# Kernel tuning notes

Measured on AMD Instinct MI355X. Metric: run time of the kernel, lower is better.

## Reference

```python
import jax, jax.numpy as jnp
import numpy as np

N_FILTERS = 40
FILTER_SIZE = 401   # int(16000*25/1000), forced odd
POOL_STRIDE = 160   # int(16000*10/1000)
EPS = 1e-6
S_SMOOTH = 0.04     # fixed PCEN smoothing coefficient s
DELTA = 2.0         # fixed PCEN bias delta
R_MIN, R_MAX = 0.2, 1.0
HIDDEN = 32


def setup_inputs() -> dict:
    key = jax.random.key(0)
    ks = jax.random.split(key, 6)
    B, L = 8, 160000
    x = jax.random.normal(ks[0], (B, L), dtype=jnp.float32)
    # mel-initialized Gabor params (as in mel_filter_params)
    sr, fmin, fmax = 16000.0, 60.0, 7800.0
    min_mel = 1127.0 * np.log1p(fmin / 700.0)
    max_mel = 1127.0 * np.log1p(fmax / 700.0)
    peaks_mel = np.linspace(min_mel, max_mel, N_FILTERS + 2)
    peaks_hz = 700.0 * np.expm1(peaks_mel / 1127.0)
    center_freqs = jnp.asarray(peaks_hz[1:-1] * 2.0 * np.pi / sr, dtype=jnp.float32)
    z = np.sqrt(2.0 * np.log(2.0)) / np.pi
    bandwidths = jnp.asarray(z * sr / (peaks_hz[2:] - peaks_hz[:-2]), dtype=jnp.float32)
    pooling_widths = jnp.full((N_FILTERS,), 0.4, dtype=jnp.float32)
    # GRU (input_size=1, hidden=32) + head Linear(32,32)->ReLU->Linear(32,2)
    def gl(k, shape):
        return jax.random.normal(k, shape, dtype=jnp.float32) * 0.1
    w_ih = gl(ks[1], (3 * HIDDEN, 1))
    w_hh = gl(ks[2], (3 * HIDDEN, HIDDEN))
    b_ih = jnp.zeros((3 * HIDDEN,), jnp.float32)
    b_hh = jnp.zeros((3 * HIDDEN,), jnp.float32)
    hw1 = gl(ks[3], (32, HIDDEN)); hb1 = jnp.zeros((32,), jnp.float32)
    hw2 = gl(ks[4], (2, 32)); hb2 = jnp.zeros((2,), jnp.float32)
    return dict(x=x, center_freqs=center_freqs, bandwidths=bandwidths,
                pooling_widths=pooling_widths, w_ih=w_ih, w_hh=w_hh,
                b_ih=b_ih, b_hh=b_hh, hw1=hw1, hb1=hb1, hw2=hw2, hb2=hb2)


def _gabor_filterbank(x, center_freqs, bandwidths, pooling_widths):
    z = np.sqrt(2.0 * np.log(2.0)) / np.pi
    cf = jnp.clip(center_freqs, 0.0, np.pi)
    bw = jnp.clip(bandwidths, 4.0 * z, FILTER_SIZE * z)
    t = jnp.arange(-(FILTER_SIZE // 2), (FILTER_SIZE + 1) // 2, dtype=jnp.float32)
    denom = 1.0 / (jnp.sqrt(2.0 * np.pi) * bw)                        # [F]
    gauss = jnp.exp(-(t[None, :] ** 2) / (2.0 * bw[:, None] ** 2))    # [F,K]
    phase = cf[:, None] * t[None, :]                                  # [F,K]
    fr = denom[:, None] * gauss * jnp.cos(phase)
    fi = denom[:, None] * gauss * jnp.sin(phase)
    filt = jnp.concatenate([fr, fi], axis=0)[:, None, :]              # [2F,1,K]
    pad = FILTER_SIZE // 2
    y = jax.lax.conv_general_dilated(x[:, None, :], filt, (1,), [(pad, pad)])
    y = y ** 2
    y = y[:, :N_FILTERS] + y[:, N_FILTERS:]                           # squared modulus [B,F,L]
    pw = jnp.clip(pooling_widths, 2.0 / FILTER_SIZE, 0.5)
    tt = jnp.arange(FILTER_SIZE, dtype=jnp.float32) / (FILTER_SIZE - 1) - 0.5
    win = jnp.exp(-0.5 * (tt[None, :] / pw[:, None]) ** 2)[:, None, :]  # [F,1,K]
    y = jax.lax.conv_general_dilated(y, win, (POOL_STRIDE,), [(pad, pad)],
                                     feature_group_count=N_FILTERS)
    return y  # [B,F,T]


def _gru_cell(h, xin, w_ih, w_hh, b_ih, b_hh):
    gi = xin @ w_ih.T + b_ih   # [N,3H]
    gh = h @ w_hh.T + b_hh
    i_r, i_z, i_n = jnp.split(gi, 3, axis=-1)
    h_r, h_z, h_n = jnp.split(gh, 3, axis=-1)
    r = jax.nn.sigmoid(i_r + h_r)
    zz = jax.nn.sigmoid(i_z + h_z)
    n = jnp.tanh(i_n + r * h_n)
    return (1.0 - zz) * n + zz * h


def _adaptive_pcen(frames, w_ih, w_hh, b_ih, b_hh, hw1, hb1, hw2, hb2):
    B, F, T = frames.shape
    Xt = jnp.transpose(frames, (2, 0, 1))  # [T,B,F]

    def controller(x_prev, x_t):  # each [B,F] -> per-bin (alpha, r)
        xp = x_prev.reshape(-1, 1)
        xc = x_t.reshape(-1, 1)
        h = jnp.zeros((B * F, HIDDEN), frames.dtype)
        h = _gru_cell(h, xp, w_ih, w_hh, b_ih, b_hh)
        h = _gru_cell(h, xc, w_ih, w_hh, b_ih, b_hh)
        hid = jax.nn.relu(h @ hw1.T + hb1)
        logits = hid @ hw2.T + hb2  # [B*F,2]
        alpha = jax.nn.sigmoid(logits[:, 0]).reshape(B, F)
        r = (R_MIN + (R_MAX - R_MIN) * jax.nn.sigmoid(logits[:, 1])).reshape(B, F)
        return alpha, r

    def step(carry, X_t):
        M_prev, X_prev = carry
        alpha, r = controller(X_prev, X_t)
        M_t = (1.0 - S_SMOOTH) * M_prev + S_SMOOTH * X_t
        out = (X_t / (M_t + EPS) ** alpha + DELTA) ** r - DELTA ** r
        return (M_t, X_t), out

    init = (jnp.zeros((B, F), frames.dtype), Xt[0])
    _, outs = jax.lax.scan(step, init, Xt)
    return jnp.transpose(outs, (1, 2, 0))  # [B,F,T]


def reference(x, center_freqs, bandwidths, pooling_widths,
              w_ih, w_hh, b_ih, b_hh, hw1, hb1, hw2, hb2):
    frames = _gabor_filterbank(x, center_freqs, bandwidths, pooling_widths)
    return _adaptive_pcen(frames, w_ih, w_hh, b_ih, b_hh, hw1, hb1, hw2, hb2)
```

## Files before the change

### kernel.cpp

```cpp
#include <hip/hip_runtime.h>
#include <math.h>

#define NF 40
#define FS 401
#define AST 424
#define PSTRIDE 160
#define BB 8
#define LL 160000
#define PADL 256
#define LST 161024
#define TOUT 1000
#define NTILE 512
#define NCHUNKC 313
#define ROWCH 121
#define ROWST (ROWCH*8)
#define EROW 520
#define TCP 16
#define NCHUNKP 63
#define NCONVB 5032

typedef __attribute__((ext_vector_type(8))) _Float16 half8v;
typedef __attribute__((ext_vector_type(4))) _Float16 half4v;
typedef __attribute__((ext_vector_type(4))) float float4v;
typedef _Float16 f16;

__device__ __forceinline__ float sigm(float x) { return 1.0f / (1.0f + __expf(-x)); }
__device__ __forceinline__ float tanh_fast(float x) { return 1.0f - 2.0f / (__expf(2.0f * x) + 1.0f); }

__global__ __launch_bounds__(256) void prep_all(
    const float* __restrict__ x, const float* __restrict__ cf_,
    const float* __restrict__ bw_, f16* __restrict__ xb, f16* __restrict__ Ag)
{
    int blk = blockIdx.x;
    if (blk < NCONVB) {
        int i = blk * 256 + threadIdx.x;
        int b = i / LST, o = i % LST;
        float v = 0.0f;
        if (o >= PADL && o < PADL + LL) v = x[b * LL + (o - PADL)];
        xb[i] = (f16)v;
        return;
    }
    const float PI_F = 3.14159265358979323846f;
    int row = blk - NCONVB;
    int f = row >> 1, comp = row & 1;
    float Z = sqrtf(2.0f * logf(2.0f)) / PI_F;
    float cf = fminf(fmaxf(cf_[f], 0.0f), PI_F);
    float bw = fminf(fmaxf(bw_[f], 4.0f * Z), 401.0f * Z);
    float denom = 1.0f / (sqrtf(2.0f * PI_F) * bw);
    float inv2 = 1.0f / (2.0f * bw * bw);
    for (int k = threadIdx.x; k < AST; k += 256) {
        float v = 0.0f;
        if (k < FS) {
            float t = (float)(k - 200);
            float g = denom * expf(-(t * t) * inv2);
            float sv, cv;
            sincosf(cf * t, &sv, &cv);
            v = comp ? g * sv : g * cv;
        }
        Ag[row * AST + k] = (f16)v;
    }
}

__global__ __launch_bounds__(256, 2) void conv_mfma(
    const f16* __restrict__ xb,
    const f16* __restrict__ Ag,
    f16* __restrict__ eb)
{
    __shared__ __align__(16) unsigned char smem[40 * EROW * 2];
    f16* slab = (f16*)smem;
    f16* eL   = (f16*)smem;

    int chunk = blockIdx.x;
    int bi = blockIdx.y;
    int p0 = chunk * NTILE;
    int pbase = PADL + p0 - 200;
    const f16* xs = xb + (size_t)bi * LST;
    int tid = threadIdx.x;

    for (int sc = tid; sc < 8 * 120; sc += 256) {
        int r = sc / 120, m = sc - r * 120;
        int s0 = pbase + 8 * m + (r & ~1);
        const uint* gp = (const uint*)(xs + s0);
        uint v0 = gp[0], v1 = gp[1], v2 = gp[2], v3 = gp[3], v4 = gp[4];
        if (r & 1) {
            v0 = __builtin_amdgcn_alignbyte(v1, v0, 2);
            v1 = __builtin_amdgcn_alignbyte(v2, v1, 2);
            v2 = __builtin_amdgcn_alignbyte(v3, v2, 2);
            v3 = __builtin_amdgcn_alignbyte(v4, v3, 2);
        }
        *(uint4*)(&slab[r * ROWST + 8 * m]) = make_uint4(v0, v1, v2, v3);
    }
    __syncthreads();

    int wv = tid >> 6, lane = tid & 63, q = lane >> 4, l15 = lane & 15;

    float4v acc[5][8];
#pragma unroll
    for (int t = 0; t < 5; ++t)
#pragma unroll
        for (int s = 0; s < 8; ++s)
            acc[t][s] = (float4v){0.f, 0.f, 0.f, 0.f};

    const f16* aP[5];
    const f16* bPtr[10];
#pragma unroll
    for (int t = 0; t < 5; ++t) aP[t] = Ag + (16 * t + l15) * AST + 8 * q;
#pragma unroll
    for (int s = 0; s < 10; ++s) {
        int pos = 128 * wv + 16 * s + l15;
        bPtr[s] = slab + (pos & 7) * ROWST + 8 * ((pos >> 3) + q);
    }

    half8v bf[8];
#pragma unroll
    for (int s = 0; s < 8; ++s) bf[s] = *(const half8v*)(bPtr[s]);

#pragma unroll
    for (int kk = 0; kk < 13; ++kk) {
        int k = 32 * kk;
        half8v af[5];
#pragma unroll
        for (int t = 0; t < 5; ++t) af[t] = *(const half8v*)(aP[t] + k);
        half8v nb0, nb1;
        if (kk < 12) {
            nb0 = *(const half8v*)(bPtr[8] + k);
            nb1 = *(const half8v*)(bPtr[9] + k);
        }
#pragma unroll
        for (int t = 0; t < 5; ++t)
#pragma unroll
            for (int s = 0; s < 8; ++s)
                acc[t][s] = __builtin_amdgcn_mfma_f32_16x16x32_f16(af[t], bf[s], acc[t][s], 0, 0, 0);
        if (kk < 12) {
#pragma unroll
            for (int s = 0; s < 6; ++s) bf[s] = bf[s + 2];
            bf[6] = nb0; bf[7] = nb1;
        }
    }

    __syncthreads();

#pragma unroll
    for (int t = 0; t < 5; ++t) {
        int f0 = 8 * t + 2 * q;
#pragma unroll
        for (int s = 0; s < 8; ++s) {
            float4v a = acc[t][s];
            int pl = 128 * wv + 16 * s + l15;
            eL[f0 * EROW + pl] = (f16)(a.x * a.x + a.y * a.y);
            eL[(f0 + 1) * EROW + pl] = (f16)(a.z * a.z + a.w * a.w);
        }
    }
    __syncthreads();

    f16* ebb = eb + (size_t)bi * NF * LL;
#pragma unroll
    for (int it = 0; it < 10; ++it) {
        int idx = it * 256 + tid;
        int row = idx >> 6;
        int off = (idx & 63) * 8;
        if (p0 + off < LL) {
            uint4 v = *(const uint4*)(&eL[row * EROW + off]);
            *(uint4*)(&ebb[row * LL + p0 + off]) = v;
        }
    }
}

__global__ __launch_bounds__(256) void pool_kernel(
    const f16* __restrict__ eb, const float* __restrict__ pw_, float* __restrict__ Xout)
{
    __shared__ float ys[2816];
    __shared__ float win[416];
    int chunk = blockIdx.x;
    int f = blockIdx.y;
    int bi = blockIdx.z;
    int tau0 = chunk * TCP;
    int start = tau0 * PSTRIDE - 200;
    int tid = threadIdx.x;

    float pw = fminf(fmaxf(pw_[f], 2.0f / 401.0f), 0.5f);
    float invpw = 1.0f / pw;
    for (int k = tid; k < 416; k += 256) {
        float w = 0.0f;
        if (k < FS) {
            float tt = (float)k * (1.0f / 400.0f) - 0.5f;
            float u = tt * invpw;
            w = expf(-0.5f * u * u);
        }
        win[k] = w;
    }
    const f16* erow = eb + ((size_t)bi * NF + f) * LL;
    if (start >= 0 && start + 2816 <= LL) {
        for (int j = tid; j < 352; j += 256) {
            half8v v = *(const half8v*)(erow + start + 8 * j);
#pragma unroll
            for (int i = 0; i < 8; ++i) ys[8 * j + i] = (float)v[i];
        }
    } else {
        for (int j = tid; j < 2816; j += 256) {
            int p = start + j;
            ys[j] = (p >= 0 && p < LL) ? (float)erow[p] : 0.0f;
        }
    }
    __syncthreads();

    int ft = tid >> 4, l16 = tid & 15;
    float acc = 0.0f;
    int yo = ft * PSTRIDE;
    for (int kw = l16; kw < FS; kw += 16)
        acc += ys[yo + kw] * win[kw];
#pragma unroll
    for (int off = 8; off > 0; off >>= 1)
        acc += __shfl_down(acc, off, 16);
    int tau = tau0 + ft;
    if (l16 == 0 && tau < TOUT)
        Xout[((size_t)bi * NF + f) * TOUT + tau] = acc;
}

__global__ __launch_bounds__(256) void pcen_scan_kernel(
    const float* __restrict__ X, float* __restrict__ M)
{
    int wid = (blockIdx.x * 256 + threadIdx.x) >> 6;
    int lane = threadIdx.x & 63;
    if (wid >= BB * NF) return;
    const float a1 = 0.96f;
    const float a2 = a1 * a1;
    const float a4 = a2 * a2;
    const float a8 = a4 * a4;
    const float a16 = a8 * a8;
    const float a32 = a16 * a16;
    const float ss = 0.04f;
    float al1 = powf(a1, (float)(lane + 1));
    float carry = 0.0f;
    const float* row = X + wid * TOUT;
    float* mrow = M + wid * TOUT;

    for (int c = 0; c < TOUT; c += 64) {
        int t = c + lane;
        float v = (t < TOUT) ? row[t] : 0.0f;
        float y = ss * v;
        float u;
        u = __shfl_up(y, 1, 64);  if (lane >= 1)  y = fmaf(a1, u, y);
        u = __shfl_up(y, 2, 64);  if (lane >= 2)  y = fmaf(a2, u, y);
        u = __shfl_up(y, 4, 64);  if (lane >= 4)  y = fmaf(a4, u, y);
        u = __shfl_up(y, 8, 64);  if (lane >= 8)  y = fmaf(a8, u, y);
        u = __shfl_up(y, 16, 64); if (lane >= 16) y = fmaf(a16, u, y);
        u = __shfl_up(y, 32, 64); if (lane >= 32) y = fmaf(a32, u, y);
        y = fmaf(al1, carry, y);
        carry = __shfl(y, 63, 64);
        if (t < TOUT) mrow[t] = y;
    }
}

__global__ __launch_bounds__(256) void pcen_ctrl_mfma(
    const float* __restrict__ X, const float* __restrict__ M,
    const float* __restrict__ w_ih, const float* __restrict__ w_hh,
    const float* __restrict__ b_ih, const float* __restrict__ b_hh,
    const float* __restrict__ hw1, const float* __restrict__ hb1,
    const float* __restrict__ hw2, const float* __restrict__ hb2,
    float* __restrict__ out)
{
    __shared__ f16 s_whhA[96 * 40];
    __shared__ f16 s_w1A[32 * 40];
    __shared__ __align__(16) float4 s_A1[32];
    __shared__ __align__(16) float4 s_A2[32];
    __shared__ float s_hb1[32];
    __shared__ float s_hw2[64];
    __shared__ float s_hb2[2];
    __shared__ f16 sh1[4][16 * 40];
    __shared__ f16 sh2[4][16 * 40];
    __shared__ float sxc[4][16], sxp[4][16], smv[4][16];

    int tid = threadIdx.x;
    for (int i = tid; i < 96 * 32; i += 256) {
        int m = i >> 5, k = i & 31;
        s_whhA[m * 40 + k] = (f16)w_hh[i];
    }
    for (int i = tid; i < 32 * 32; i += 256) {
        int m = i >> 5, k = i & 31;
        s_w1A[m * 40 + k] = (f16)hw1[i];
    }
    if (tid < 32) {
        int j = tid;
        s_A1[j] = make_float4(w_ih[j], b_ih[j] + b_hh[j],
                              w_ih[32 + j], b_ih[32 + j] + b_hh[32 + j]);
        s_A2[j] = make_float4(w_ih[64 + j], b_ih[64 + j], b_hh[64 + j], 0.0f);
        s_hb1[j] = hb1[j];
    }
    if (tid < 64) s_hw2[tid] = hw2[tid];
    if (tid < 2)  s_hb2[tid] = hb2[tid];
    __syncthreads();

    int wv = tid >> 6, lane = tid & 63;
    int c = lane & 15, q = lane >> 4;
    int instBase = blockIdx.x * 64 + wv * 16;

    if (lane < 16) {
        int idx = instBase + lane;
        int t = idx % TOUT;
        float xcv = X[idx];
        float xpv = (t == 0) ? xcv : X[idx - 1];
        sxc[wv][lane] = xcv;
        sxp[wv][lane] = xpv;
        smv[wv][lane] = M[idx];
    }
    float xp = sxp[wv][c];
    float xc = sxc[wv][c];
    float mv = smv[wv][c];

    float h1v[8];
#pragma unroll
    for (int jj = 0; jj < 8; ++jj) {
        int j = (jj < 4) ? (4 * q + jj) : (16 + 4 * q + (jj - 4));
        float4 a1 = s_A1[j];
        float4 a2 = s_A2[j];
        float r = sigm(fmaf(xp, a1.x, a1.y));
        float z = sigm(fmaf(xp, a1.z, a1.w));
        float n = tanh_fast(fmaf(xp, a2.x, a2.y) + r * a2.z);
        h1v[jj] = (1.0f - z) * n;
    }

    {
        half4v lo = {(f16)h1v[0], (f16)h1v[1], (f16)h1v[2], (f16)h1v[3]};
        half4v hi = {(f16)h1v[4], (f16)h1v[5], (f16)h1v[6], (f16)h1v[7]};
        *(half4v*)(&sh1[wv][c * 40 + 4 * q]) = lo;
        *(half4v*)(&sh1[wv][c * 40 + 16 + 4 * q]) = hi;
    }

    float4v acc[6];
    {
        half8v bf = *(const half8v*)(&sh1[wv][c * 40 + 8 * q]);
#pragma unroll
        for (int t = 0; t < 6; ++t) {
            half8v af = *(const half8v*)(&s_whhA[(16 * t + c) * 40 + 8 * q]);
            acc[t] = __builtin_amdgcn_mfma_f32_16x16x32_f16(af, bf, (float4v){0.f,0.f,0.f,0.f}, 0, 0, 0);
        }
    }

    float h2v[8];
#pragma unroll
    for (int jj = 0; jj < 8; ++jj) {
        int j = (jj < 4) ? (4 * q + jj) : (16 + 4 * q + (jj - 4));
        int reg = jj & 3;
        float accR = (jj < 4) ? acc[0][reg] : acc[1][reg];
        float accZ = (jj < 4) ? acc[2][reg] : acc[3][reg];
        float accN = (jj < 4) ? acc[4][reg] : acc[5][reg];
        float4 a1 = s_A1[j];
        float4 a2 = s_A2[j];
        float r = sigm(fmaf(xc, a1.x, a1.y) + accR);
        float z = sigm(fmaf(xc, a1.z, a1.w) + accZ);
        float gn = accN + a2.z;
        float n = tanh_fast(fmaf(xc, a2.x, a2.y) + r * gn);
        h2v[jj] = fmaf(z, h1v[jj] - n, n);
    }

    {
        half4v lo = {(f16)h2v[0], (f16)h2v[1], (f16)h2v[2], (f16)h2v[3]};
        half4v hi = {(f16)h2v[4], (f16)h2v[5], (f16)h2v[6], (f16)h2v[7]};
        *(half4v*)(&sh2[wv][c * 40 + 4 * q]) = lo;
        *(half4v*)(&sh2[wv][c * 40 + 16 + 4 * q]) = hi;
    }

    float4v hacc[2];
    {
        half8v bf = *(const half8v*)(&sh2[wv][c * 40 + 8 * q]);
#pragma unroll
        for (int t = 0; t < 2; ++t) {
            half8v af = *(const half8v*)(&s_w1A[(16 * t + c) * 40 + 8 * q]);
            hacc[t] = __builtin_amdgcn_mfma_f32_16x16x32_f16(af, bf, (float4v){0.f,0.f,0.f,0.f}, 0, 0, 0);
        }
    }

    float p0 = 0.f, p1 = 0.f;
#pragma unroll
    for (int jj = 0; jj < 8; ++jj) {
        int i = (jj < 4) ? (4 * q + jj) : (16 + 4 * q + (jj - 4));
        int reg = jj & 3;
        float hv = (jj < 4) ? hacc[0][reg] : hacc[1][reg];
        hv = fmaxf(hv + s_hb1[i], 0.0f);
        p0 = fmaf(hv, s_hw2[i], p0);
        p1 = fmaf(hv, s_hw2[32 + i], p1);
    }
    p0 += __shfl_xor(p0, 16);
    p0 += __shfl_xor(p0, 32);
    p1 += __shfl_xor(p1, 16);
    p1 += __shfl_xor(p1, 32);

    float alpha = sigm(p0 + s_hb2[0]);
    float rr = fmaf(0.8f, sigm(p1 + s_hb2[1]), 0.2f);
    float md = __expf(alpha * __logf(mv + 1e-6f));
    float bse = xc / md + 2.0f;
    float val = __expf(rr * __logf(bse)) - __expf(rr * 0.69314718056f);
    if (lane < 16)
        out[instBase + lane] = val;
}

extern "C" void kernel_launch(void* const* d_in, const int* in_sizes, int n_in,
                              void* d_out, int out_size, void* d_ws, size_t ws_size,
                              hipStream_t stream) {
    const float* x    = (const float*)d_in[0];
    const float* cf   = (const float*)d_in[1];
    const float* bw   = (const float*)d_in[2];
    const float* pw   = (const float*)d_in[3];
    const float* w_ih = (const float*)d_in[4];
    const float* w_hh = (const float*)d_in[5];
    const float* b_ih = (const float*)d_in[6];
    const float* b_hh = (const float*)d_in[7];
    const float* hw1  = (const float*)d_in[8];
    const float* hb1  = (const float*)d_in[9];
    const float* hw2  = (const float*)d_in[10];
    const float* hb2  = (const float*)d_in[11];
    float* out = (float*)d_out;

    const size_t xb_b = (size_t)BB * LST * 2;
    const size_t ag_b = (size_t)80 * AST * 2;
    const size_t xm_b = (size_t)2 * BB * NF * TOUT * 4;
    size_t fixed = xb_b + ag_b + xm_b;
    size_t e_per_batch = (size_t)NF * LL * 2;
    int nb;
    if (ws_size >= fixed + 8 * e_per_batch)      nb = 8;
    else if (ws_size >= fixed + 2 * e_per_batch) nb = 2;
    else                                         nb = 1;
    int nslice = BB / nb;

    f16* xb   = (f16*)d_ws;
    f16* Ag   = xb + (size_t)BB * LST;
    f16* ebuf = Ag + (size_t)80 * AST;
    float* Xf = (float*)(ebuf + (size_t)nb * NF * LL);
    float* Mf = Xf + (size_t)BB * NF * TOUT;

    prep_all<<<dim3(NCONVB + 80), dim3(256), 0, stream>>>(x, cf, bw, xb, Ag);

    for (int sl = 0; sl < nslice; ++sl) {
        conv_mfma<<<dim3(NCHUNKC, nb), dim3(256), 0, stream>>>(
            xb + (size_t)sl * nb * LST, Ag, ebuf);
        pool_kernel<<<dim3(NCHUNKP, NF, nb), dim3(256), 0, stream>>>(
            ebuf, pw, Xf + (size_t)sl * nb * NF * TOUT);
    }

    pcen_scan_kernel<<<dim3((BB * NF * 64) / 256), dim3(256), 0, stream>>>(Xf, Mf);
    pcen_ctrl_mfma<<<dim3((BB * NF * TOUT) / 64), dim3(256), 0, stream>>>(
        Xf, Mf, w_ih, w_hh, b_ih, b_hh, hw1, hb1, hw2, hb2, out);
}
```

Before: 260.7 us.

## Precompute pooling windows, keep pooling tiles in f16, batch more work per block

Gaussian pooling windows are now computed once per filter in the prep kernel instead of in every pooling block. The pool kernel stages the energy tile in shared memory as f16 rather than expanded float, and each block now covers 32 frames using paired half2/float2 loads. The PCEN controller kernel now handles four 16-instance groups per wave in a loop, which cuts the launch to a quarter of the blocks and amortises the shared-memory weight setup. The cost is more serial work per block and one extra small workspace buffer.

```diff
diff --git a/kernel.cpp b/kernel.cpp
--- a/kernel.cpp
+++ b/kernel.cpp
@@ -15,12 +15,15 @@
 #define ROWCH 121
 #define ROWST (ROWCH*8)
 #define EROW 520
-#define TCP 16
-#define NCHUNKP 63
+#define TCP 32
+#define NCHUNKP 32
+#define PELEM (TCP*PSTRIDE + 408)
+#define WROW 402
 #define NCONVB 5032
 
 typedef __attribute__((ext_vector_type(8))) _Float16 half8v;
 typedef __attribute__((ext_vector_type(4))) _Float16 half4v;
+typedef __attribute__((ext_vector_type(2))) _Float16 half2v;
 typedef __attribute__((ext_vector_type(4))) float float4v;
 typedef _Float16 f16;
 
@@ -29,7 +32,8 @@
 
 __global__ __launch_bounds__(256) void prep_all(
     const float* __restrict__ x, const float* __restrict__ cf_,
-    const float* __restrict__ bw_, f16* __restrict__ xb, f16* __restrict__ Ag)
+    const float* __restrict__ bw_, const float* __restrict__ pw_,
+    f16* __restrict__ xb, f16* __restrict__ Ag, float* __restrict__ winG)
 {
     int blk = blockIdx.x;
     if (blk < NCONVB) {
@@ -41,23 +45,38 @@
         return;
     }
     const float PI_F = 3.14159265358979323846f;
-    int row = blk - NCONVB;
-    int f = row >> 1, comp = row & 1;
-    float Z = sqrtf(2.0f * logf(2.0f)) / PI_F;
-    float cf = fminf(fmaxf(cf_[f], 0.0f), PI_F);
-    float bw = fminf(fmaxf(bw_[f], 4.0f * Z), 401.0f * Z);
-    float denom = 1.0f / (sqrtf(2.0f * PI_F) * bw);
-    float inv2 = 1.0f / (2.0f * bw * bw);
-    for (int k = threadIdx.x; k < AST; k += 256) {
-        float v = 0.0f;
-        if (k < FS) {
-            float t = (float)(k - 200);
-            float g = denom * expf(-(t * t) * inv2);
-            float sv, cv;
-            sincosf(cf * t, &sv, &cv);
-            v = comp ? g * sv : g * cv;
-        }
-        Ag[row * AST + k] = (f16)v;
+    if (blk < NCONVB + 80) {
+        int row = blk - NCONVB;
+        int f = row >> 1, comp = row & 1;
+        float Z = sqrtf(2.0f * logf(2.0f)) / PI_F;
+        float cf = fminf(fmaxf(cf_[f], 0.0f), PI_F);
+        float bw = fminf(fmaxf(bw_[f], 4.0f * Z), 401.0f * Z);
+        float denom = 1.0f / (sqrtf(2.0f * PI_F) * bw);
+        float inv2 = 1.0f / (2.0f * bw * bw);
+        for (int k = threadIdx.x; k < AST; k += 256) {
+            float v = 0.0f;
+            if (k < FS) {
+                float t = (float)(k - 200);
+                float g = denom * expf(-(t * t) * inv2);
+                float sv, cv;
+                sincosf(cf * t, &sv, &cv);
+                v = comp ? g * sv : g * cv;
+            }
+            Ag[row * AST + k] = (f16)v;
+        }
+        return;
+    }
+    int f = blk - NCONVB - 80;
+    float pw = fminf(fmaxf(pw_[f], 2.0f / 401.0f), 0.5f);
+    float invpw = 1.0f / pw;
+    for (int j = threadIdx.x; j < WROW; j += 256) {
+        float w = 0.0f;
+        if (j < FS) {
+            float tt = (float)j * (1.0f / 400.0f) - 0.5f;
+            float u = tt * invpw;
+            w = expf(-0.5f * u * u);
+        }
+        winG[f * WROW + j] = w;
     }
 }
 
@@ -167,10 +186,10 @@
 }
 
 __global__ __launch_bounds__(256) void pool_kernel(
-    const f16* __restrict__ eb, const float* __restrict__ pw_, float* __restrict__ Xout)
+    const f16* __restrict__ eb, const float* __restrict__ winG, float* __restrict__ Xout)
 {
-    __shared__ float ys[2816];
-    __shared__ float win[416];
+    __shared__ __align__(16) f16 es[PELEM + 8];
+    __shared__ __align__(16) float win[416];
     int chunk = blockIdx.x;
     int f = blockIdx.y;
     int bi = blockIdx.z;
@@ -178,43 +197,42 @@
     int start = tau0 * PSTRIDE - 200;
     int tid = threadIdx.x;
 
-    float pw = fminf(fmaxf(pw_[f], 2.0f / 401.0f), 0.5f);
-    float invpw = 1.0f / pw;
-    for (int k = tid; k < 416; k += 256) {
-        float w = 0.0f;
-        if (k < FS) {
-            float tt = (float)k * (1.0f / 400.0f) - 0.5f;
-            float u = tt * invpw;
-            w = expf(-0.5f * u * u);
-        }
-        win[k] = w;
-    }
+    for (int k = tid; k < 416; k += 256)
+        win[k] = (k < WROW) ? winG[f * WROW + k] : 0.0f;
+
     const f16* erow = eb + ((size_t)bi * NF + f) * LL;
-    if (start >= 0 && start + 2816 <= LL) {
-        for (int j = tid; j < 352; j += 256) {
-            half8v v = *(const half8v*)(erow + start + 8 * j);
-#pragma unroll
-            for (int i = 0; i < 8; ++i) ys[8 * j + i] = (float)v[i];
-        }
+    if (start >= 0 && start + PELEM <= LL) {
+        for (int j = tid; j < PELEM / 8; j += 256)
+            *(uint4*)(&es[8 * j]) = *(const uint4*)(erow + start + 8 * j);
     } else {
-        for (int j = tid; j < 2816; j += 256) {
+        for (int j = tid; j < PELEM; j += 256) {
             int p = start + j;
-            ys[j] = (p >= 0 && p < LL) ? (float)erow[p] : 0.0f;
+            es[j] = (p >= 0 && p < LL) ? erow[p] : (f16)0.0f;
         }
     }
     __syncthreads();
 
     int ft = tid >> 4, l16 = tid & 15;
-    float acc = 0.0f;
-    int yo = ft * PSTRIDE;
-    for (int kw = l16; kw < FS; kw += 16)
-        acc += ys[yo + kw] * win[kw];
-#pragma unroll
-    for (int off = 8; off > 0; off >>= 1)
-        acc += __shfl_down(acc, off, 16);
-    int tau = tau0 + ft;
-    if (l16 == 0 && tau < TOUT)
-        Xout[((size_t)bi * NF + f) * TOUT + tau] = acc;
+#pragma unroll
+    for (int pass = 0; pass < 2; ++pass) {
+        int frame = pass * 16 + ft;
+        int base = frame * PSTRIDE;
+        float acc = 0.0f;
+#pragma unroll
+        for (int m = 0; m < 13; ++m) {
+            int kw = 2 * l16 + 32 * m;
+            half2v ep = *(const half2v*)(&es[base + kw]);
+            float2 wp = *(const float2*)(&win[kw]);
+            acc = fmaf((float)ep[0], wp.x, acc);
+            acc = fmaf((float)ep[1], wp.y, acc);
+        }
+#pragma unroll
+        for (int off = 8; off > 0; off >>= 1)
+            acc += __shfl_down(acc, off, 16);
+        int tau = tau0 + frame;
+        if (l16 == 0 && tau < TOUT)
+            Xout[((size_t)bi * NF + f) * TOUT + tau] = acc;
+    }
 }
 
 __global__ __launch_bounds__(256) void pcen_scan_kernel(
@@ -269,7 +287,6 @@
     __shared__ float s_hb2[2];
     __shared__ f16 sh1[4][16 * 40];
     __shared__ f16 sh2[4][16 * 40];
-    __shared__ float sxc[4][16], sxp[4][16], smv[4][16];
 
     int tid = threadIdx.x;
     for (int i = tid; i < 96 * 32; i += 256) {
@@ -293,106 +310,103 @@
 
     int wv = tid >> 6, lane = tid & 63;
     int c = lane & 15, q = lane >> 4;
-    int instBase = blockIdx.x * 64 + wv * 16;
-
-    if (lane < 16) {
-        int idx = instBase + lane;
-        int t = idx % TOUT;
-        float xcv = X[idx];
-        float xpv = (t == 0) ? xcv : X[idx - 1];
-        sxc[wv][lane] = xcv;
-        sxp[wv][lane] = xpv;
-        smv[wv][lane] = M[idx];
-    }
-    float xp = sxp[wv][c];
-    float xc = sxc[wv][c];
-    float mv = smv[wv][c];
-
-    float h1v[8];
-#pragma unroll
-    for (int jj = 0; jj < 8; ++jj) {
-        int j = (jj < 4) ? (4 * q + jj) : (16 + 4 * q + (jj - 4));
-        float4 a1 = s_A1[j];
-        float4 a2 = s_A2[j];
-        float r = sigm(fmaf(xp, a1.x, a1.y));
-        float z = sigm(fmaf(xp, a1.z, a1.w));
-        float n = tanh_fast(fmaf(xp, a2.x, a2.y) + r * a2.z);
-        h1v[jj] = (1.0f - z) * n;
-    }
-
-    {
-        half4v lo = {(f16)h1v[0], (f16)h1v[1], (f16)h1v[2], (f16)h1v[3]};
-        half4v hi = {(f16)h1v[4], (f16)h1v[5], (f16)h1v[6], (f16)h1v[7]};
-        *(half4v*)(&sh1[wv][c * 40 + 4 * q]) = lo;
-        *(half4v*)(&sh1[wv][c * 40 + 16 + 4 * q]) = hi;
-    }
-
-    float4v acc[6];
-    {
-        half8v bf = *(const half8v*)(&sh1[wv][c * 40 + 8 * q]);
-#pragma unroll
-        for (int t = 0; t < 6; ++t) {
-            half8v af = *(const half8v*)(&s_whhA[(16 * t + c) * 40 + 8 * q]);
-            acc[t] = __builtin_amdgcn_mfma_f32_16x16x32_f16(af, bf, (float4v){0.f,0.f,0.f,0.f}, 0, 0, 0);
-        }
-    }
-
-    float h2v[8];
-#pragma unroll
-    for (int jj = 0; jj < 8; ++jj) {
-        int j = (jj < 4) ? (4 * q + jj) : (16 + 4 * q + (jj - 4));
-        int reg = jj & 3;
-        float accR = (jj < 4) ? acc[0][reg] : acc[1][reg];
-        float accZ = (jj < 4) ? acc[2][reg] : acc[3][reg];
-        float accN = (jj < 4) ? acc[4][reg] : acc[5][reg];
-        float4 a1 = s_A1[j];
-        float4 a2 = s_A2[j];
-        float r = sigm(fmaf(xc, a1.x, a1.y) + accR);
-        float z = sigm(fmaf(xc, a1.z, a1.w) + accZ);
-        float gn = accN + a2.z;
-        float n = tanh_fast(fmaf(xc, a2.x, a2.y) + r * gn);
-        h2v[jj] = fmaf(z, h1v[jj] - n, n);
-    }
-
-    {
-        half4v lo = {(f16)h2v[0], (f16)h2v[1], (f16)h2v[2], (f16)h2v[3]};
-        half4v hi = {(f16)h2v[4], (f16)h2v[5], (f16)h2v[6], (f16)h2v[7]};
-        *(half4v*)(&sh2[wv][c * 40 + 4 * q]) = lo;
-        *(half4v*)(&sh2[wv][c * 40 + 16 + 4 * q]) = hi;
-    }
-
-    float4v hacc[2];
-    {
-        half8v bf = *(const half8v*)(&sh2[wv][c * 40 + 8 * q]);
-#pragma unroll
-        for (int t = 0; t < 2; ++t) {
-            half8v af = *(const half8v*)(&s_w1A[(16 * t + c) * 40 + 8 * q]);
-            hacc[t] = __builtin_amdgcn_mfma_f32_16x16x32_f16(af, bf, (float4v){0.f,0.f,0.f,0.f}, 0, 0, 0);
-        }
-    }
-
-    float p0 = 0.f, p1 = 0.f;
-#pragma unroll
-    for (int jj = 0; jj < 8; ++jj) {
-        int i = (jj < 4) ? (4 * q + jj) : (16 + 4 * q + (jj - 4));
-        int reg = jj & 3;
-        float hv = (jj < 4) ? hacc[0][reg] : hacc[1][reg];
-        hv = fmaxf(hv + s_hb1[i], 0.0f);
-        p0 = fmaf(hv, s_hw2[i], p0);
-        p1 = fmaf(hv, s_hw2[32 + i], p1);
-    }
-    p0 += __shfl_xor(p0, 16);
-    p0 += __shfl_xor(p0, 32);
-    p1 += __shfl_xor(p1, 16);
-    p1 += __shfl_xor(p1, 32);
-
-    float alpha = sigm(p0 + s_hb2[0]);
-    float rr = fmaf(0.8f, sigm(p1 + s_hb2[1]), 0.2f);
-    float md = __expf(alpha * __logf(mv + 1e-6f));
-    float bse = xc / md + 2.0f;
-    float val = __expf(rr * __logf(bse)) - __expf(rr * 0.69314718056f);
-    if (lane < 16)
-        out[instBase + lane] = val;
+    int waveBase = blockIdx.x * 256 + wv * 64;
+
+#pragma unroll
+    for (int g = 0; g < 4; ++g) {
+        int idx0 = waveBase + g * 16;
+        int idxc = idx0 + c;
+        int tt0 = idx0 % TOUT + c;
+        float xc = X[idxc];
+        float xp = (tt0 == 0 || tt0 == TOUT) ? xc : X[idxc - 1];
+        float mv = M[idxc];
+
+        float h1v[8];
+#pragma unroll
+        for (int jj = 0; jj < 8; ++jj) {
+            int j = (jj < 4) ? (4 * q + jj) : (16 + 4 * q + (jj - 4));
+            float4 a1 = s_A1[j];
+            float4 a2 = s_A2[j];
+            float r = sigm(fmaf(xp, a1.x, a1.y));
+            float z = sigm(fmaf(xp, a1.z, a1.w));
+            float n = tanh_fast(fmaf(xp, a2.x, a2.y) + r * a2.z);
+            h1v[jj] = (1.0f - z) * n;
+        }
+
+        {
+            half4v lo = {(f16)h1v[0], (f16)h1v[1], (f16)h1v[2], (f16)h1v[3]};
+            half4v hi = {(f16)h1v[4], (f16)h1v[5], (f16)h1v[6], (f16)h1v[7]};
+            *(half4v*)(&sh1[wv][c * 40 + 4 * q]) = lo;
+            *(half4v*)(&sh1[wv][c * 40 + 16 + 4 * q]) = hi;
+        }
+
+        float4v acc[6];
+        {
+            half8v bfv = *(const half8v*)(&sh1[wv][c * 40 + 8 * q]);
+#pragma unroll
+            for (int t = 0; t < 6; ++t) {
+                half8v af = *(const half8v*)(&s_whhA[(16 * t + c) * 40 + 8 * q]);
+                acc[t] = __builtin_amdgcn_mfma_f32_16x16x32_f16(af, bfv, (float4v){0.f,0.f,0.f,0.f}, 0, 0, 0);
+            }
+        }
+
+        float h2v[8];
+#pragma unroll
+        for (int jj = 0; jj < 8; ++jj) {
+            int j = (jj < 4) ? (4 * q + jj) : (16 + 4 * q + (jj - 4));
+            int reg = jj & 3;
+            float accR = (jj < 4) ? acc[0][reg] : acc[1][reg];
+            float accZ = (jj < 4) ? acc[2][reg] : acc[3][reg];
+            float accN = (jj < 4) ? acc[4][reg] : acc[5][reg];
+            float4 a1 = s_A1[j];
+            float4 a2 = s_A2[j];
+            float r = sigm(fmaf(xc, a1.x, a1.y) + accR);
+            float z = sigm(fmaf(xc, a1.z, a1.w) + accZ);
+            float gn = accN + a2.z;
+            float n = tanh_fast(fmaf(xc, a2.x, a2.y) + r * gn);
+            h2v[jj] = fmaf(z, h1v[jj] - n, n);
+        }
+
+        {
+            half4v lo = {(f16)h2v[0], (f16)h2v[1], (f16)h2v[2], (f16)h2v[3]};
+            half4v hi = {(f16)h2v[4], (f16)h2v[5], (f16)h2v[6], (f16)h2v[7]};
+            *(half4v*)(&sh2[wv][c * 40 + 4 * q]) = lo;
+            *(half4v*)(&sh2[wv][c * 40 + 16 + 4 * q]) = hi;
+        }
+
+        float4v hacc[2];
+        {
+            half8v bfv = *(const half8v*)(&sh2[wv][c * 40 + 8 * q]);
+#pragma unroll
+            for (int t = 0; t < 2; ++t) {
+                half8v af = *(const half8v*)(&s_w1A[(16 * t + c) * 40 + 8 * q]);
+                hacc[t] = __builtin_amdgcn_mfma_f32_16x16x32_f16(af, bfv, (float4v){0.f,0.f,0.f,0.f}, 0, 0, 0);
+            }
+        }
+
+        float p0 = 0.f, p1 = 0.f;
+#pragma unroll
+        for (int jj = 0; jj < 8; ++jj) {
+            int i = (jj < 4) ? (4 * q + jj) : (16 + 4 * q + (jj - 4));
+            int reg = jj & 3;
+            float hv = (jj < 4) ? hacc[0][reg] : hacc[1][reg];
+            hv = fmaxf(hv + s_hb1[i], 0.0f);
+            p0 = fmaf(hv, s_hw2[i], p0);
+            p1 = fmaf(hv, s_hw2[32 + i], p1);
+        }
+        p0 += __shfl_xor(p0, 16);
+        p0 += __shfl_xor(p0, 32);
+        p1 += __shfl_xor(p1, 16);
+        p1 += __shfl_xor(p1, 32);
+
+        float alpha = sigm(p0 + s_hb2[0]);
+        float rr = fmaf(0.8f, sigm(p1 + s_hb2[1]), 0.2f);
+        float md = __expf(alpha * __logf(mv + 1e-6f));
+        float bse = xc / md + 2.0f;
+        float val = __expf(rr * __logf(bse)) - __expf(rr * 0.69314718056f);
+        if (q == 0)
+            out[idxc] = val;
+    }
 }
 
 extern "C" void kernel_launch(void* const* d_in, const int* in_sizes, int n_in,
@@ -414,8 +428,9 @@
 
     const size_t xb_b = (size_t)BB * LST * 2;
     const size_t ag_b = (size_t)80 * AST * 2;
+    const size_t wg_b = (size_t)NF * WROW * 4;
     const size_t xm_b = (size_t)2 * BB * NF * TOUT * 4;
-    size_t fixed = xb_b + ag_b + xm_b;
+    size_t fixed = xb_b + ag_b + wg_b + xm_b;
     size_t e_per_batch = (size_t)NF * LL * 2;
     int nb;
     if (ws_size >= fixed + 8 * e_per_batch)      nb = 8;
@@ -423,22 +438,23 @@
     else                                         nb = 1;
     int nslice = BB / nb;
 
-    f16* xb   = (f16*)d_ws;
-    f16* Ag   = xb + (size_t)BB * LST;
-    f16* ebuf = Ag + (size_t)80 * AST;
-    float* Xf = (float*)(ebuf + (size_t)nb * NF * LL);
-    float* Mf = Xf + (size_t)BB * NF * TOUT;
-
-    prep_all<<<dim3(NCONVB + 80), dim3(256), 0, stream>>>(x, cf, bw, xb, Ag);
+    f16* xb    = (f16*)d_ws;
+    f16* Ag    = xb + (size_t)BB * LST;
+    float* winG = (float*)(Ag + (size_t)80 * AST);
+    f16* ebuf  = (f16*)(winG + (size_t)NF * WROW);
+    float* Xf  = (float*)(ebuf + (size_t)nb * NF * LL);
+    float* Mf  = Xf + (size_t)BB * NF * TOUT;
+
+    prep_all<<<dim3(NCONVB + 80 + NF), dim3(256), 0, stream>>>(x, cf, bw, pw, xb, Ag, winG);
 
     for (int sl = 0; sl < nslice; ++sl) {
         conv_mfma<<<dim3(NCHUNKC, nb), dim3(256), 0, stream>>>(
             xb + (size_t)sl * nb * LST, Ag, ebuf);
         pool_kernel<<<dim3(NCHUNKP, NF, nb), dim3(256), 0, stream>>>(
-            ebuf, pw, Xf + (size_t)sl * nb * NF * TOUT);
+            ebuf, winG, Xf + (size_t)sl * nb * NF * TOUT);
     }
 
     pcen_scan_kernel<<<dim3((BB * NF * 64) / 256), dim3(256), 0, stream>>>(Xf, Mf);
-    pcen_ctrl_mfma<<<dim3((BB * NF * TOUT) / 64), dim3(256), 0, stream>>>(
+    pcen_ctrl_mfma<<<dim3((BB * NF * TOUT) / 256), dim3(256), 0, stream>>>(
         Xf, Mf, w_ih, w_hh, b_ih, b_hh, hw1, hb1, hw2, hb2, out);
 }
```

Result: no change. 265.9 us (+2.0%).
